# Kernel tuning notes

Measured on AMD Instinct MI355X. Metric: run time of the kernel, lower is better.

The kernel has to match this reference:

```python
import jax, jax.numpy as jnp
import numpy as np

THRESHOLD = 0.5
T = 16777216  # 2**24 timesteps
PERIOD = 256  # note every 256 frames
NOTE_LEN = 200  # offset 200 frames after onset


def setup_inputs() -> dict:
    key = jax.random.key(0)
    k_u, k_e = jax.random.split(key)
    u = jax.random.normal(k_u, (T, 2), dtype=jnp.float32)
    e = jax.random.normal(k_e, (T, 2), dtype=jnp.float32)
    phase = jnp.arange(T, dtype=jnp.int32) % PERIOD
    onsets = (phase == 0).astype(jnp.int32)
    offsets = (phase == NOTE_LEN).astype(jnp.int32)
    return {"u": u, "e": e, "onsets": onsets, "offsets": offsets}


def reference(u, e, onsets, offsets):
    # Vectorized equivalent of the sequential mask build: a timestep is inside
    # a note iff the number of onsets seen so far (inclusive) exceeds the
    # number of offsets seen so far (inclusive). Per-note mask columns are
    # disjoint, so the stacked (T, n_notes) mask reduces to this 1D active mask
    # for both the thresholded count and the normalizer sum(mask).
    cum_on = jnp.cumsum(onsets)
    cum_off = jnp.cumsum(offsets)
    active = (cum_on > cum_off).astype(u.dtype)  # (T,)
    u_f0 = u[:, 0]  # x[0].split(1, -1) -> first channel is f0
    e_f0 = e[:, 0]
    diff = jnp.abs(active * (e_f0 - u_f0))  # mask*|e-u| since mask in {0,1}
    loss = jnp.sum((diff > THRESHOLD).astype(u.dtype)) / jnp.sum(active)
    return loss
```

## Files before the change

### kernel.cpp

```cpp
#include <hip/hip_runtime.h>
#include <math.h>

constexpr int T_TOTAL = 16777216;
constexpr int TPB     = 256;
constexpr int SEG     = 2048;
constexpr int NSEG    = T_TOTAL / SEG;
constexpr int NBLK    = NSEG / 4;
constexpr int ITERS   = SEG / 128;
constexpr float THRESHOLD = 0.5f;

__global__ void __launch_bounds__(TPB)
k_segsums(const int2* __restrict__ on2, const int2* __restrict__ off2,
          int* __restrict__ segsums) {
    const int lane = threadIdx.x & 63;
    const int wid  = threadIdx.x >> 6;
    const int seg  = blockIdx.x * 4 + wid;
    const int base = seg * (SEG / 2);
    int s = 0;
    #pragma unroll
    for (int it = 0; it < ITERS; ++it) {
        int2 a = on2[base + it * 64 + lane];
        int2 c = off2[base + it * 64 + lane];
        s += a.x + a.y - c.x - c.y;
    }
    #pragma unroll
    for (int d = 32; d > 0; d >>= 1) s += __shfl_xor(s, d);
    if (lane == 0) segsums[seg] = s;
}

__global__ void __launch_bounds__(TPB)
k_scan(int* __restrict__ segsums) {
    __shared__ int wsum[4];
    const int lane = threadIdx.x & 63;
    const int wid  = threadIdx.x >> 6;
    int vals[NSEG / TPB];
    const int base = threadIdx.x * (NSEG / TPB);
    int s = 0;
    #pragma unroll
    for (int i = 0; i < NSEG / TPB; i++) { vals[i] = segsums[base + i]; s += vals[i]; }
    int x = s;
    #pragma unroll
    for (int d = 1; d < 64; d <<= 1) {
        int y = __shfl_up(x, d);
        if (lane >= d) x += y;
    }
    if (lane == 63) wsum[wid] = x;
    __syncthreads();
    int wbase = 0;
    #pragma unroll
    for (int w = 0; w < 3; w++) if (w < wid) wbase += wsum[w];
    int ex = wbase + (x - s);
    #pragma unroll
    for (int i = 0; i < NSEG / TPB; i++) { int v = vals[i]; segsums[base + i] = ex; ex += v; }
}

__global__ void __launch_bounds__(TPB)
k_count(const int2* __restrict__ on2, const int2* __restrict__ off2,
        const float4* __restrict__ u4, const float4* __restrict__ e4,
        const int* __restrict__ segpre, int2* __restrict__ partials) {
    const int lane = threadIdx.x & 63;
    const int wid  = threadIdx.x >> 6;
    const int seg  = blockIdx.x * 4 + wid;
    const int base = seg * (SEG / 2);
    const unsigned long long le = (~0ull) >> (63 - lane);
    const unsigned long long lt = le >> 1;

    int basep = segpre[seg];
    int cover = 0, cact = 0;

    #pragma unroll 4
    for (int it = 0; it < ITERS; ++it) {
        const int idx = base + it * 64 + lane;
        int2   a  = on2[idx];
        int2   c  = off2[idx];
        float4 uv = u4[idx];
        float4 ev = e4[idx];

        unsigned long long be_on  = __ballot(a.x != 0);
        unsigned long long bo_on  = __ballot(a.y != 0);
        unsigned long long be_off = __ballot(c.x != 0);
        unsigned long long bo_off = __ballot(c.y != 0);

        const int de = __popcll(be_on & le) - __popcll(be_off & le);
        const int pe = basep + de + __popcll(bo_on & lt) - __popcll(bo_off & lt);
        const int po = basep + de + __popcll(bo_on & le) - __popcll(bo_off & le);
        basep += __popcll(be_on) - __popcll(be_off)
               + __popcll(bo_on) - __popcll(bo_off);

        const int a0 = pe > 0, a1 = po > 0;
        cact += a0 + a1;
        if (a0 && fabsf(ev.x - uv.x) > THRESHOLD) cover++;
        if (a1 && fabsf(ev.z - uv.z) > THRESHOLD) cover++;
    }

    #pragma unroll
    for (int d = 32; d > 0; d >>= 1) {
        cover += __shfl_xor(cover, d);
        cact  += __shfl_xor(cact, d);
    }
    __shared__ int sc[4], sa[4];
    if (lane == 0) { sc[wid] = cover; sa[wid] = cact; }
    __syncthreads();
    if (threadIdx.x == 0)
        partials[blockIdx.x] = make_int2(sc[0] + sc[1] + sc[2] + sc[3],
                                         sa[0] + sa[1] + sa[2] + sa[3]);
}

__global__ void __launch_bounds__(TPB)
k_final(const int2* __restrict__ partials, float* __restrict__ out) {
    const int lane = threadIdx.x & 63;
    const int wid  = threadIdx.x >> 6;
    int c = 0, a = 0;
    for (int i = threadIdx.x; i < NBLK; i += TPB) {
        int2 p = partials[i];
        c += p.x; a += p.y;
    }
    #pragma unroll
    for (int d = 32; d > 0; d >>= 1) {
        c += __shfl_xor(c, d);
        a += __shfl_xor(a, d);
    }
    __shared__ int sc[4], sa[4];
    if (lane == 0) { sc[wid] = c; sa[wid] = a; }
    __syncthreads();
    if (threadIdx.x == 0) {
        float ctot = (float)(sc[0] + sc[1] + sc[2] + sc[3]);
        float atot = (float)(sa[0] + sa[1] + sa[2] + sa[3]);
        out[0] = ctot / atot;
    }
}

extern "C" void kernel_launch(void* const* d_in, const int* in_sizes, int n_in,
                              void* d_out, int out_size, void* d_ws, size_t ws_size,
                              hipStream_t stream) {
    const float* u   = (const float*)d_in[0];
    const float* e   = (const float*)d_in[1];
    const int*   on  = (const int*)d_in[2];
    const int*   off = (const int*)d_in[3];

    int*  segsums  = (int*)d_ws;
    int2* partials = (int2*)(segsums + NSEG);

    k_segsums<<<NBLK, TPB, 0, stream>>>((const int2*)on, (const int2*)off, segsums);
    k_scan<<<1, TPB, 0, stream>>>(segsums);
    k_count<<<NBLK, TPB, 0, stream>>>((const int2*)on, (const int2*)off,
                                      (const float4*)u, (const float4*)e,
                                      segsums, partials);
    k_final<<<1, TPB, 0, stream>>>(partials, (float*)d_out);
}
```

Baseline: 93.76 us.

## Fuse data read into single pass by compacting ballots, then scan compact bitmasks

```diff
diff --git a/kernel.cpp b/kernel.cpp
--- a/kernel.cpp
+++ b/kernel.cpp
@@ -1,5 +1,7 @@
 #include <hip/hip_runtime.h>
 #include <math.h>
+
+typedef unsigned long long u64;
 
 constexpr int T_TOTAL = 16777216;
 constexpr int TPB     = 256;
@@ -7,67 +9,19 @@
 constexpr int NSEG    = T_TOTAL / SEG;
 constexpr int NBLK    = NSEG / 4;
 constexpr int ITERS   = SEG / 128;
+constexpr int BWRD    = 6;
 constexpr float THRESHOLD = 0.5f;
 
-__global__ void __launch_bounds__(TPB)
-k_segsums(const int2* __restrict__ on2, const int2* __restrict__ off2,
-          int* __restrict__ segsums) {
+
+__global__ void __launch_bounds__(TPB)
+k_prep(const int2* __restrict__ on2, const int2* __restrict__ off2,
+       const float4* __restrict__ u4, const float4* __restrict__ e4,
+       u64* __restrict__ ballots, int* __restrict__ segsums) {
     const int lane = threadIdx.x & 63;
     const int wid  = threadIdx.x >> 6;
     const int seg  = blockIdx.x * 4 + wid;
     const int base = seg * (SEG / 2);
-    int s = 0;
-    #pragma unroll
-    for (int it = 0; it < ITERS; ++it) {
-        int2 a = on2[base + it * 64 + lane];
-        int2 c = off2[base + it * 64 + lane];
-        s += a.x + a.y - c.x - c.y;
-    }
-    #pragma unroll
-    for (int d = 32; d > 0; d >>= 1) s += __shfl_xor(s, d);
-    if (lane == 0) segsums[seg] = s;
-}
-
-__global__ void __launch_bounds__(TPB)
-k_scan(int* __restrict__ segsums) {
-    __shared__ int wsum[4];
-    const int lane = threadIdx.x & 63;
-    const int wid  = threadIdx.x >> 6;
-    int vals[NSEG / TPB];
-    const int base = threadIdx.x * (NSEG / TPB);
-    int s = 0;
-    #pragma unroll
-    for (int i = 0; i < NSEG / TPB; i++) { vals[i] = segsums[base + i]; s += vals[i]; }
-    int x = s;
-    #pragma unroll
-    for (int d = 1; d < 64; d <<= 1) {
-        int y = __shfl_up(x, d);
-        if (lane >= d) x += y;
-    }
-    if (lane == 63) wsum[wid] = x;
-    __syncthreads();
-    int wbase = 0;
-    #pragma unroll
-    for (int w = 0; w < 3; w++) if (w < wid) wbase += wsum[w];
-    int ex = wbase + (x - s);
-    #pragma unroll
-    for (int i = 0; i < NSEG / TPB; i++) { int v = vals[i]; segsums[base + i] = ex; ex += v; }
-}
-
-__global__ void __launch_bounds__(TPB)
-k_count(const int2* __restrict__ on2, const int2* __restrict__ off2,
-        const float4* __restrict__ u4, const float4* __restrict__ e4,
-        const int* __restrict__ segpre, int2* __restrict__ partials) {
-    const int lane = threadIdx.x & 63;
-    const int wid  = threadIdx.x >> 6;
-    const int seg  = blockIdx.x * 4 + wid;
-    const int base = seg * (SEG / 2);
-    const unsigned long long le = (~0ull) >> (63 - lane);
-    const unsigned long long lt = le >> 1;
-
-    int basep = segpre[seg];
-    int cover = 0, cact = 0;
-
+    int ssum = 0;
     #pragma unroll 4
     for (int it = 0; it < ITERS; ++it) {
         const int idx = base + it * 64 + lane;
@@ -75,24 +29,141 @@
         int2   c  = off2[idx];
         float4 uv = u4[idx];
         float4 ev = e4[idx];
-
-        unsigned long long be_on  = __ballot(a.x != 0);
-        unsigned long long bo_on  = __ballot(a.y != 0);
-        unsigned long long be_off = __ballot(c.x != 0);
-        unsigned long long bo_off = __ballot(c.y != 0);
-
+        u64 pos_e  = __ballot(a.x > c.x);
+        u64 neg_e  = __ballot(c.x > a.x);
+        u64 pos_o  = __ballot(a.y > c.y);
+        u64 neg_o  = __ballot(c.y > a.y);
+        u64 over_e = __ballot(fabsf(ev.x - uv.x) > THRESHOLD);
+        u64 over_o = __ballot(fabsf(ev.z - uv.z) > THRESHOLD);
+        ssum += __popcll(pos_e) - __popcll(neg_e)
+              + __popcll(pos_o) - __popcll(neg_o);
+        u64 v = pos_e;
+        v = (lane == 1) ? neg_e  : v;
+        v = (lane == 2) ? pos_o  : v;
+        v = (lane == 3) ? neg_o  : v;
+        v = (lane == 4) ? over_e : v;
+        v = (lane == 5) ? over_o : v;
+        if (lane < BWRD) ballots[(size_t)(seg * ITERS + it) * BWRD + lane] = v;
+    }
+    if (lane == 0) segsums[seg] = ssum;
+}
+
+__global__ void __launch_bounds__(TPB)
+k_scan(int* __restrict__ segsums) {
+    __shared__ int wsum[4];
+    const int lane = threadIdx.x & 63;
+    const int wid  = threadIdx.x >> 6;
+    int vals[NSEG / TPB];
+    const int base = threadIdx.x * (NSEG / TPB);
+    int s = 0;
+    #pragma unroll
+    for (int i = 0; i < NSEG / TPB; i++) { vals[i] = segsums[base + i]; s += vals[i]; }
+    int x = s;
+    #pragma unroll
+    for (int d = 1; d < 64; d <<= 1) {
+        int y = __shfl_up(x, d);
+        if (lane >= d) x += y;
+    }
+    if (lane == 63) wsum[wid] = x;
+    __syncthreads();
+    int wbase = 0;
+    #pragma unroll
+    for (int w = 0; w < 3; w++) if (w < wid) wbase += wsum[w];
+    int ex = wbase + (x - s);
+    #pragma unroll
+    for (int i = 0; i < NSEG / TPB; i++) { int v = vals[i]; segsums[base + i] = ex; ex += v; }
+}
+
+__global__ void __launch_bounds__(TPB)
+k_count2(const u64* __restrict__ ballots, const int* __restrict__ segpre,
+         int2* __restrict__ partials) {
+    const int lane = threadIdx.x & 63;
+    const int wid  = threadIdx.x >> 6;
+    const int seg  = blockIdx.x * 4 + wid;
+    const u64 le = (~0ull) >> (63 - lane);
+    const u64 lt = le >> 1;
+    int basep = segpre[seg];
+    int cover = 0, cact = 0;
+    const ulonglong2* bb = (const ulonglong2*)(ballots + (size_t)seg * ITERS * BWRD);
+    #pragma unroll 4
+    for (int it = 0; it < ITERS; ++it) {
+        ulonglong2 w0 = bb[it * 3 + 0];
+        ulonglong2 w1 = bb[it * 3 + 1];
+        ulonglong2 w2 = bb[it * 3 + 2];
+        const int de = __popcll(w0.x & le) - __popcll(w0.y & le);
+        const int pe = basep + de + __popcll(w1.x & lt) - __popcll(w1.y & lt);
+        const int po = basep + de + __popcll(w1.x & le) - __popcll(w1.y & le);
+        basep += __popcll(w0.x) - __popcll(w0.y)
+               + __popcll(w1.x) - __popcll(w1.y);
+        const int a0 = pe > 0, a1 = po > 0;
+        cact += a0 + a1;
+        cover += (a0 & (int)((w2.x >> lane) & 1)) + (a1 & (int)((w2.y >> lane) & 1));
+    }
+    #pragma unroll
+    for (int d = 32; d > 0; d >>= 1) {
+        cover += __shfl_xor(cover, d);
+        cact  += __shfl_xor(cact, d);
+    }
+    __shared__ int sc[4], sa[4];
+    if (lane == 0) { sc[wid] = cover; sa[wid] = cact; }
+    __syncthreads();
+    if (threadIdx.x == 0)
+        partials[blockIdx.x] = make_int2(sc[0] + sc[1] + sc[2] + sc[3],
+                                         sa[0] + sa[1] + sa[2] + sa[3]);
+}
+
+__global__ void __launch_bounds__(TPB)
+k_segsums(const int2* __restrict__ on2, const int2* __restrict__ off2,
+          int* __restrict__ segsums) {
+    const int lane = threadIdx.x & 63;
+    const int wid  = threadIdx.x >> 6;
+    const int seg  = blockIdx.x * 4 + wid;
+    const int base = seg * (SEG / 2);
+    int s = 0;
+    #pragma unroll
+    for (int it = 0; it < ITERS; ++it) {
+        int2 a = on2[base + it * 64 + lane];
+        int2 c = off2[base + it * 64 + lane];
+        s += a.x + a.y - c.x - c.y;
+    }
+    #pragma unroll
+    for (int d = 32; d > 0; d >>= 1) s += __shfl_xor(s, d);
+    if (lane == 0) segsums[seg] = s;
+}
+
+__global__ void __launch_bounds__(TPB)
+k_count(const int2* __restrict__ on2, const int2* __restrict__ off2,
+        const float4* __restrict__ u4, const float4* __restrict__ e4,
+        const int* __restrict__ segpre, int2* __restrict__ partials) {
+    const int lane = threadIdx.x & 63;
+    const int wid  = threadIdx.x >> 6;
+    const int seg  = blockIdx.x * 4 + wid;
+    const int base = seg * (SEG / 2);
+    const u64 le = (~0ull) >> (63 - lane);
+    const u64 lt = le >> 1;
+    int basep = segpre[seg];
+    int cover = 0, cact = 0;
+    #pragma unroll 4
+    for (int it = 0; it < ITERS; ++it) {
+        const int idx = base + it * 64 + lane;
+        int2   a  = on2[idx];
+        int2   c  = off2[idx];
+        float4 uv = u4[idx];
+        float4 ev = e4[idx];
+        u64 be_on  = __ballot(a.x != 0);
+        u64 bo_on  = __ballot(a.y != 0);
+        u64 be_off = __ballot(c.x != 0);
+        u64 bo_off = __ballot(c.y != 0);
         const int de = __popcll(be_on & le) - __popcll(be_off & le);
         const int pe = basep + de + __popcll(bo_on & lt) - __popcll(bo_off & lt);
         const int po = basep + de + __popcll(bo_on & le) - __popcll(bo_off & le);
         basep += __popcll(be_on) - __popcll(be_off)
                + __popcll(bo_on) - __popcll(bo_off);
-
         const int a0 = pe > 0, a1 = po > 0;
         cact += a0 + a1;
         if (a0 && fabsf(ev.x - uv.x) > THRESHOLD) cover++;
         if (a1 && fabsf(ev.z - uv.z) > THRESHOLD) cover++;
     }
-
     #pragma unroll
     for (int d = 32; d > 0; d >>= 1) {
         cover += __shfl_xor(cover, d);
@@ -140,11 +211,22 @@
 
     int*  segsums  = (int*)d_ws;
     int2* partials = (int2*)(segsums + NSEG);
-
-    k_segsums<<<NBLK, TPB, 0, stream>>>((const int2*)on, (const int2*)off, segsums);
-    k_scan<<<1, TPB, 0, stream>>>(segsums);
-    k_count<<<NBLK, TPB, 0, stream>>>((const int2*)on, (const int2*)off,
-                                      (const float4*)u, (const float4*)e,
-                                      segsums, partials);
+    u64*  ballots  = (u64*)((char*)d_ws + 48 * 1024);
+
+    const size_t need = 48 * 1024 + (size_t)NSEG * ITERS * BWRD * sizeof(u64);
+
+    if (ws_size >= need) {
+        k_prep<<<NBLK, TPB, 0, stream>>>((const int2*)on, (const int2*)off,
+                                         (const float4*)u, (const float4*)e,
+                                         ballots, segsums);
+        k_scan<<<1, TPB, 0, stream>>>(segsums);
+        k_count2<<<NBLK, TPB, 0, stream>>>(ballots, segsums, partials);
+    } else {
+        k_segsums<<<NBLK, TPB, 0, stream>>>((const int2*)on, (const int2*)off, segsums);
+        k_scan<<<1, TPB, 0, stream>>>(segsums);
+        k_count<<<NBLK, TPB, 0, stream>>>((const int2*)on, (const int2*)off,
+                                          (const float4*)u, (const float4*)e,
+                                          segsums, partials);
+    }
     k_final<<<1, TPB, 0, stream>>>(partials, (float*)d_out);
 }
```

New measurement: 105.0 us. +12.0%, slower.
